# Performance work log

Measured on AMD Instinct MI355X. Metric: run time of the kernel, lower is better.

Reference implementation:

```python
import jax, jax.numpy as jnp
import numpy as np

DIM = 768
HEADS = 12
DIM_HEAD = 64
INNER = HEADS * DIM_HEAD  # 768
EPS = 1e-5


def setup_inputs() -> dict:
    key = jax.random.key(0)
    ks = jax.random.split(key, 5)
    x = jax.random.normal(ks[0], (4, 2048, DIM), dtype=jnp.float32)
    ln_g = jnp.ones((DIM,), dtype=jnp.float32)
    ln_b = jnp.zeros((DIM,), dtype=jnp.float32)
    s1 = 1.0 / np.sqrt(DIM)
    W_qkv = jax.random.uniform(ks[1], (DIM, 3 * INNER), dtype=jnp.float32, minval=-s1, maxval=s1)
    b_qkv = jax.random.uniform(ks[2], (3 * INNER,), dtype=jnp.float32, minval=-s1, maxval=s1)
    s2 = 1.0 / np.sqrt(INNER)
    W_out = jax.random.uniform(ks[3], (INNER, DIM), dtype=jnp.float32, minval=-s2, maxval=s2)
    b_out = jax.random.uniform(ks[4], (DIM,), dtype=jnp.float32, minval=-s2, maxval=s2)
    return {"x": x, "ln_g": ln_g, "ln_b": ln_b, "W_qkv": W_qkv, "b_qkv": b_qkv, "W_out": W_out, "b_out": b_out}


def reference(x, ln_g, ln_b, W_qkv, b_qkv, W_out, b_out):
    b, n, _ = x.shape
    # pre-norm LayerNorm
    mu = jnp.mean(x, axis=-1, keepdims=True)
    var = jnp.mean(jnp.square(x - mu), axis=-1, keepdims=True)
    xn = (x - mu) * jax.lax.rsqrt(var + EPS) * ln_g + ln_b
    qkv = xn @ W_qkv + b_qkv  # [b, n, 3*inner]
    q, k, v = jnp.split(qkv, 3, axis=-1)
    def to_heads(t):
        return t.reshape(b, n, HEADS, DIM_HEAD).transpose(0, 2, 1, 3)  # b h n d
    q, k, v = map(to_heads, (q, k, v))
    q = q * (DIM_HEAD ** -0.5)
    sim = jnp.einsum('bhid,bhjd->bhij', q, k)
    attn = jax.nn.softmax(sim, axis=-1)  # dropout is identity (p=0.0)
    out = jnp.einsum('bhij,bhjd->bhid', attn, v)
    out = out.transpose(0, 2, 1, 3).reshape(b, n, INNER)
    return out @ W_out + b_out
```

## Files before the change

### kernel.cpp

```cpp
#include <hip/hip_runtime.h>
#include <cstdint>
#include <cstddef>


#define SEQ    2048
#define NBATCH 4
#define DMODEL 768
#define NHEADS 12
#define DHEAD  64
#define MROWS  (NBATCH * SEQ)
#define NQKV   (3 * DMODEL)
#define KT     64
#define NT     (SEQ / KT)

using f32x4  = __attribute__((ext_vector_type(4))) float;
using u16x8  = __attribute__((ext_vector_type(8))) unsigned short;
using s16x8  = __attribute__((ext_vector_type(8))) short;

__device__ __forceinline__ unsigned short f2bf(float f) {
  union { float f; unsigned int u; } x; x.f = f;
  unsigned int r = x.u + 0x7fffu + ((x.u >> 16) & 1u);
  return (unsigned short)(r >> 16);
}

#if defined(__has_builtin)
#if __has_builtin(__builtin_amdgcn_cvt_pk_bf16_f32)
#define HAVE_PK_BF16 1
#endif
#if __has_builtin(__builtin_amdgcn_exp2f)
#define HAVE_EXP2 1
#endif
#endif

__device__ __forceinline__ unsigned int pk_bf16(float a, float b) {
#ifdef HAVE_PK_BF16
  auto v = __builtin_amdgcn_cvt_pk_bf16_f32(a, b);
  union { decltype(v) v2; unsigned int u; } c; c.v2 = v; return c.u;
#else
  return (unsigned int)f2bf(a) | ((unsigned int)f2bf(b) << 16);
#endif
}

__device__ __forceinline__ float fexp2(float x) {
#ifdef HAVE_EXP2
  return __builtin_amdgcn_exp2f(x);
#else
  return exp2f(x);
#endif
}

__device__ __forceinline__ f32x4 mfma16(u16x8 a, u16x8 b, f32x4 c) {
  return __builtin_amdgcn_mfma_f32_16x16x32_bf16((s16x8)a, (s16x8)b, c, 0, 0, 0);
}

__device__ __forceinline__ void gl_lds16(const void* g, void* l) {
  __builtin_amdgcn_global_load_lds(
      (const __attribute__((address_space(1))) void*)g,
      (__attribute__((address_space(3))) void*)l, 16, 0, 0);
}

__global__ __launch_bounds__(256) void ln_kernel(
    const float* __restrict__ x, const float* __restrict__ g,
    const float* __restrict__ bb, unsigned short* __restrict__ xn) {
  __shared__ float red[8];
  const int row = blockIdx.x, t = threadIdx.x;
  const float* xr = x + (size_t)row * DMODEL;
  float v0 = xr[t], v1 = xr[t + 256], v2 = xr[t + 512];
  float s = v0 + v1 + v2;
#pragma unroll
  for (int o = 32; o; o >>= 1) s += __shfl_down(s, o);
  if ((t & 63) == 0) red[t >> 6] = s;
  __syncthreads();
  float mu = (red[0] + red[1] + red[2] + red[3]) * (1.0f / DMODEL);
  float d0 = v0 - mu, d1 = v1 - mu, d2 = v2 - mu;
  float q = d0 * d0 + d1 * d1 + d2 * d2;
#pragma unroll
  for (int o = 32; o; o >>= 1) q += __shfl_down(q, o);
  if ((t & 63) == 0) red[4 + (t >> 6)] = q;
  __syncthreads();
  float var = (red[4] + red[5] + red[6] + red[7]) * (1.0f / DMODEL);
  float rstd = rsqrtf(var + 1e-5f);
  size_t base = (size_t)row * DMODEL;
  xn[base + t]       = f2bf(d0 * rstd * g[t]       + bb[t]);
  xn[base + t + 256] = f2bf(d1 * rstd * g[t + 256] + bb[t + 256]);
  xn[base + t + 512] = f2bf(d2 * rstd * g[t + 512] + bb[t + 512]);
}

__global__ __launch_bounds__(256) void tconv_kernel(
    const float* __restrict__ W, unsigned short* __restrict__ Wt, int N) {
  __shared__ float tile[32][33];
  const int n0 = blockIdx.x * 32, k0 = blockIdx.y * 32;
  const int tx = threadIdx.x & 31, ty = threadIdx.x >> 5;
#pragma unroll
  for (int r = 0; r < 4; ++r)
    tile[ty + r * 8][tx] = W[(size_t)(k0 + ty + r * 8) * N + n0 + tx];
  __syncthreads();
#pragma unroll
  for (int r = 0; r < 4; ++r)
    Wt[(size_t)(n0 + ty + r * 8) * DMODEL + k0 + tx] = f2bf(tile[tx][ty + r * 8]);
}

__global__ __launch_bounds__(256, 2) void gemm_qk_kernel(
    const unsigned short* __restrict__ Wt, const unsigned short* __restrict__ xn,
    const float* __restrict__ bias, unsigned short* __restrict__ qb,
    unsigned short* __restrict__ kb) {
  __shared__ alignas(16) unsigned short As[128 * 64];
  __shared__ alignas(16) unsigned short Bs[128 * 64];
  const int t = threadIdx.x, wid = t >> 6, l = t & 63, quad = l >> 4, ll = l & 15;
  const int a0 = blockIdx.x * 128;
  const int b0 = blockIdx.y * 128;
  const int wa = (wid >> 1) * 64, wb = (wid & 1) * 64;
  const int srow = l >> 3, sblk = (l & 7) ^ srow;
  f32x4 acc[4][4] = {};
  for (int k0 = 0; k0 < DMODEL; k0 += 64) {
#pragma unroll
    for (int cc = 0; cc < 4; ++cc) {
      int call = wid * 4 + cc;
      int r = call * 8 + srow;
      gl_lds16(Wt + (size_t)(a0 + r) * DMODEL + k0 + sblk * 8, &As[call * 512]);
      gl_lds16(xn + (size_t)(b0 + r) * DMODEL + k0 + sblk * 8, &Bs[call * 512]);
    }
    __syncthreads();
#pragma unroll
    for (int ks = 0; ks < 2; ++ks) {
      u16x8 af[4], bf[4];
#pragma unroll
      for (int i = 0; i < 4; ++i) {
        int ra = wa + i * 16 + ll, rb = wb + i * 16 + ll;
        int blk = (ks * 4 + quad) ^ (ll & 7);
        af[i] = *(const u16x8*)&As[ra * 64 + blk * 8];
        bf[i] = *(const u16x8*)&Bs[rb * 64 + blk * 8];
      }
#pragma unroll
      for (int mi = 0; mi < 4; ++mi)
#pragma unroll
        for (int ni = 0; ni < 4; ++ni)
          acc[mi][ni] = mfma16(af[mi], bf[ni], acc[mi][ni]);
    }
    __syncthreads();
  }
  const bool isq = (a0 < DMODEL);
  unsigned short* dst = isq ? qb : kb;
  const float sc = isq ? 0.18033688f : 1.0f;
#pragma unroll
  for (int mi = 0; mi < 4; ++mi) {
    int row0 = a0 + wa + mi * 16 + quad * 4;
    float4 bv = *(const float4*)&bias[row0];
    int rr = isq ? row0 : row0 - DMODEL;
    int h = rr >> 6, d0 = rr & 63;
#pragma unroll
    for (int ni = 0; ni < 4; ++ni) {
      int seq = b0 + wb + ni * 16 + ll;
      int b = seq >> 11, i = seq & 2047;
      uint2 pk;
      pk.x = pk_bf16((acc[mi][ni][0] + bv.x) * sc, (acc[mi][ni][1] + bv.y) * sc);
      pk.y = pk_bf16((acc[mi][ni][2] + bv.z) * sc, (acc[mi][ni][3] + bv.w) * sc);
      *(uint2*)&dst[(size_t)((b * NHEADS + h) * SEQ + i) * DHEAD + d0] = pk;
    }
  }
}

__global__ __launch_bounds__(256, 2) void gemm_v_kernel(
    const unsigned short* __restrict__ A, const unsigned short* __restrict__ Bt,
    const float* __restrict__ bias, unsigned short* __restrict__ vt) {
  __shared__ alignas(16) unsigned short As[128 * 64];
  __shared__ alignas(16) unsigned short Bs[128 * 64];
  const int t = threadIdx.x, wid = t >> 6, l = t & 63, quad = l >> 4, ll = l & 15;
  const int m0 = blockIdx.x * 128;
  const int n0 = 2 * DMODEL + blockIdx.y * 128;
  const int wm = (wid >> 1) * 64, wn = (wid & 1) * 64;
  const int srow = l >> 3, sblk = (l & 7) ^ srow;
  f32x4 acc[4][4] = {};
  for (int k0 = 0; k0 < DMODEL; k0 += 64) {
#pragma unroll
    for (int cc = 0; cc < 4; ++cc) {
      int call = wid * 4 + cc;
      int r = call * 8 + srow;
      gl_lds16(A  + (size_t)(m0 + r) * DMODEL + k0 + sblk * 8, &As[call * 512]);
      gl_lds16(Bt + (size_t)(n0 + r) * DMODEL + k0 + sblk * 8, &Bs[call * 512]);
    }
    __syncthreads();
#pragma unroll
    for (int ks = 0; ks < 2; ++ks) {
      u16x8 af[4], bf[4];
#pragma unroll
      for (int i = 0; i < 4; ++i) {
        int ra = wm + i * 16 + ll, rb = wn + i * 16 + ll;
        int blk = (ks * 4 + quad) ^ (ll & 7);
        af[i] = *(const u16x8*)&As[ra * 64 + blk * 8];
        bf[i] = *(const u16x8*)&Bs[rb * 64 + blk * 8];
      }
#pragma unroll
      for (int mi = 0; mi < 4; ++mi)
#pragma unroll
        for (int ni = 0; ni < 4; ++ni)
          acc[mi][ni] = mfma16(af[mi], bf[ni], acc[mi][ni]);
    }
    __syncthreads();
  }
#pragma unroll
  for (int mi = 0; mi < 4; ++mi) {
    int gm = m0 + wm + mi * 16 + quad * 4;
    int b = gm >> 11, i0 = gm & 2047;
#pragma unroll
    for (int ni = 0; ni < 4; ++ni) {
      int gn = n0 + wn + ni * 16 + ll;
      float bv = bias[gn];
      int rem = gn - 2 * DMODEL;
      int h = rem >> 6, d = rem & 63;
      int bh = b * NHEADS + h;
      uint2 pk;
      pk.x = pk_bf16(acc[mi][ni][0] + bv, acc[mi][ni][1] + bv);
      pk.y = pk_bf16(acc[mi][ni][2] + bv, acc[mi][ni][3] + bv);
      *(uint2*)&vt[((size_t)bh * DHEAD + d) * SEQ + i0] = pk;
    }
  }
}

__global__ __launch_bounds__(256, 3) void attn_kernel(
    const unsigned short* __restrict__ qbuf, const unsigned short* __restrict__ kbuf,
    const unsigned short* __restrict__ vtg, unsigned short* __restrict__ ao) {
  __shared__ alignas(16) unsigned short stage[2][2][KT * DHEAD];
  __shared__ alignas(16) unsigned short Pws[4][32 * 72];
  const int t = threadIdx.x, wid = t >> 6, l = t & 63, quad = l >> 4, ll = l & 15;
  const int qt = blockIdx.x, bh = blockIdx.y;
  const unsigned short* qg  = qbuf + ((size_t)bh * SEQ + qt * 128) * DHEAD;
  const unsigned short* kg0 = kbuf + (size_t)bh * SEQ * DHEAD;
  const unsigned short* vt0 = vtg  + (size_t)bh * DHEAD * SEQ;
  const int srow = l >> 3;
  const int sblk = (l & 7) ^ srow;

  unsigned short* Qs = &stage[0][0][0];
#pragma unroll
  for (int cc = 0; cc < 4; ++cc) {
    int call = wid * 4 + cc;
    gl_lds16(qg + (call * 8 + srow) * 64 + sblk * 8, Qs + call * 512);
  }
  __syncthreads();
  u16x8 qf[2][2];
#pragma unroll
  for (int mi = 0; mi < 2; ++mi)
#pragma unroll
    for (int ks = 0; ks < 2; ++ks) {
      int r = wid * 32 + mi * 16 + ll;
      int blk = (ks * 4 + quad) ^ (ll & 7);
      qf[mi][ks] = *(const u16x8*)&Qs[r * 64 + blk * 8];
    }
  __syncthreads();

  auto stage_tile = [&](int buf, int kt2) {
    const unsigned short* kg = kg0 + (size_t)kt2 * KT * DHEAD;
#pragma unroll
    for (int c = 0; c < 2; ++c) {
      int call = wid * 2 + c;
      int r = call * 8 + srow;
      gl_lds16(kg + r * 64 + sblk * 8, &stage[buf][0][call * 512]);
      gl_lds16(vt0 + (size_t)r * SEQ + kt2 * KT + sblk * 8, &stage[buf][1][call * 512]);
    }
  };

  f32x4 oacc[2][4] = {};
  float lsum[2] = {0.f, 0.f};
  unsigned short* Pw = Pws[wid];

  stage_tile(0, 0);
  int buf = 0;
  for (int kt2 = 0; kt2 < NT; ++kt2) {
    __syncthreads();
    if (kt2 + 1 < NT) stage_tile(buf ^ 1, kt2 + 1);
    const unsigned short* Ks = &stage[buf][0][0];
    const unsigned short* Vs = &stage[buf][1][0];

    f32x4 st[2][4] = {};
#pragma unroll
    for (int ks = 0; ks < 2; ++ks)
#pragma unroll
      for (int ni = 0; ni < 4; ++ni) {
        int r = ni * 16 + ll;
        int blk = (ks * 4 + quad) ^ (ll & 7);
        u16x8 kf = *(const u16x8*)&Ks[r * 64 + blk * 8];
        st[0][ni] = mfma16(kf, qf[0][ks], st[0][ni]);
        st[1][ni] = mfma16(kf, qf[1][ks], st[1][ni]);
      }

#pragma unroll
    for (int mi = 0; mi < 2; ++mi)
#pragma unroll
      for (int ni = 0; ni < 4; ++ni) {
        float p0 = fexp2(st[mi][ni][0]);
        float p1 = fexp2(st[mi][ni][1]);
        float p2 = fexp2(st[mi][ni][2]);
        float p3 = fexp2(st[mi][ni][3]);
        lsum[mi] += (p0 + p1) + (p2 + p3);
        uint2 pk;
        pk.x = pk_bf16(p0, p1);
        pk.y = pk_bf16(p2, p3);
        *(uint2*)&Pw[(mi * 16 + ll) * 72 + ni * 16 + quad * 4] = pk;
      }
    asm volatile("s_waitcnt lgkmcnt(0)" ::: "memory");

#pragma unroll
    for (int ks = 0; ks < 2; ++ks) {
      u16x8 pf0 = *(const u16x8*)&Pw[(ll) * 72 + ks * 32 + quad * 8];
      u16x8 pf1 = *(const u16x8*)&Pw[(16 + ll) * 72 + ks * 32 + quad * 8];
#pragma unroll
      for (int di = 0; di < 4; ++di) {
        int r = di * 16 + ll;
        int blk = (ks * 4 + quad) ^ (ll & 7);
        u16x8 vf = *(const u16x8*)&Vs[r * 64 + blk * 8];
        oacc[0][di] = mfma16(pf0, vf, oacc[0][di]);
        oacc[1][di] = mfma16(pf1, vf, oacc[1][di]);
      }
    }
    buf ^= 1;
  }

  float lsF[2];
#pragma unroll
  for (int mi = 0; mi < 2; ++mi) {
    float ls = lsum[mi];
    ls += __shfl_xor(ls, 16);
    ls += __shfl_xor(ls, 32);
    lsF[mi] = ls;
  }

  const int b = bh / NHEADS, h = bh - b * NHEADS;
#pragma unroll
  for (int mi = 0; mi < 2; ++mi) {
#pragma unroll
    for (int r = 0; r < 4; ++r) {
      float inv = 1.0f / __shfl(lsF[mi], quad * 4 + r);
      int row = qt * 128 + wid * 32 + mi * 16 + quad * 4 + r;
      size_t base = ((size_t)(b * SEQ + row)) * DMODEL + h * DHEAD;
#pragma unroll
      for (int di = 0; di < 4; ++di)
        ao[base + di * 16 + ll] = f2bf(oacc[mi][di][r] * inv);
    }
  }
}

__global__ __launch_bounds__(256, 2) void gemm_out_kernel(
    const unsigned short* __restrict__ Wt, const unsigned short* __restrict__ ao,
    const float* __restrict__ bias, float* __restrict__ out) {
  __shared__ alignas(16) unsigned short As[128 * 64];
  __shared__ alignas(16) unsigned short Bs[128 * 64];
  const int t = threadIdx.x, wid = t >> 6, l = t & 63, quad = l >> 4, ll = l & 15;
  const int a0 = blockIdx.x * 128;
  const int b0 = blockIdx.y * 128;
  const int wa = (wid >> 1) * 64, wb = (wid & 1) * 64;
  const int srow = l >> 3, sblk = (l & 7) ^ srow;
  f32x4 acc[4][4] = {};
  for (int k0 = 0; k0 < DMODEL; k0 += 64) {
#pragma unroll
    for (int cc = 0; cc < 4; ++cc) {
      int call = wid * 4 + cc;
      int r = call * 8 + srow;
      gl_lds16(Wt + (size_t)(a0 + r) * DMODEL + k0 + sblk * 8, &As[call * 512]);
      gl_lds16(ao + (size_t)(b0 + r) * DMODEL + k0 + sblk * 8, &Bs[call * 512]);
    }
    __syncthreads();
#pragma unroll
    for (int ks = 0; ks < 2; ++ks) {
      u16x8 af[4], bf[4];
#pragma unroll
      for (int i = 0; i < 4; ++i) {
        int ra = wa + i * 16 + ll, rb = wb + i * 16 + ll;
        int blk = (ks * 4 + quad) ^ (ll & 7);
        af[i] = *(const u16x8*)&As[ra * 64 + blk * 8];
        bf[i] = *(const u16x8*)&Bs[rb * 64 + blk * 8];
      }
#pragma unroll
      for (int mi = 0; mi < 4; ++mi)
#pragma unroll
        for (int ni = 0; ni < 4; ++ni)
          acc[mi][ni] = mfma16(af[mi], bf[ni], acc[mi][ni]);
    }
    __syncthreads();
  }
#pragma unroll
  for (int mi = 0; mi < 4; ++mi) {
    int row0 = a0 + wa + mi * 16 + quad * 4;
    float4 bv = *(const float4*)&bias[row0];
#pragma unroll
    for (int ni = 0; ni < 4; ++ni) {
      int seq = b0 + wb + ni * 16 + ll;
      float4 o;
      o.x = acc[mi][ni][0] + bv.x;
      o.y = acc[mi][ni][1] + bv.y;
      o.z = acc[mi][ni][2] + bv.z;
      o.w = acc[mi][ni][3] + bv.w;
      *(float4*)&out[(size_t)seq * DMODEL + row0] = o;
    }
  }
}

extern "C" void kernel_launch(void* const* d_in, const int* in_sizes, int n_in,
                              void* d_out, int out_size, void* d_ws, size_t ws_size,
                              hipStream_t stream) {
  const float* x     = (const float*)d_in[0];
  const float* ln_g  = (const float*)d_in[1];
  const float* ln_b  = (const float*)d_in[2];
  const float* W_qkv = (const float*)d_in[3];
  const float* b_qkv = (const float*)d_in[4];
  const float* W_out = (const float*)d_in[5];
  const float* b_out = (const float*)d_in[6];
  float* out = (float*)d_out;

  char* ws = (char*)d_ws;
  unsigned short* xn    = (unsigned short*)(ws);
  unsigned short* wqkvt = (unsigned short*)(ws + 12582912);
  unsigned short* woutt = (unsigned short*)(ws + 16121856);
  unsigned short* qb    = (unsigned short*)(ws + 17301504);
  unsigned short* kb    = (unsigned short*)(ws + 29884416);
  unsigned short* vt    = (unsigned short*)(ws + 42467328);
  unsigned short* ao    = xn;

  ln_kernel<<<MROWS, 256, 0, stream>>>(x, ln_g, ln_b, xn);
  tconv_kernel<<<dim3(NQKV / 32, DMODEL / 32), 256, 0, stream>>>(W_qkv, wqkvt, NQKV);
  tconv_kernel<<<dim3(DMODEL / 32, DMODEL / 32), 256, 0, stream>>>(W_out, woutt, DMODEL);
  gemm_qk_kernel<<<dim3(12, 64), 256, 0, stream>>>(wqkvt, xn, b_qkv, qb, kb);
  gemm_v_kernel<<<dim3(64, 6), 256, 0, stream>>>(xn, wqkvt, b_qkv, vt);
  attn_kernel<<<dim3(SEQ / 128, NBATCH * NHEADS), 256, 0, stream>>>(qb, kb, vt, ao);
  gemm_out_kernel<<<dim3(6, 64), 256, 0, stream>>>(woutt, ao, b_out, out);
}
```

Before: 240.2 us.

## Merge weight transposes and QKV GEMMs, reorder attention grid, shrink out-proj tile

The two weight transpose-convert launches become one kernel that picks its source by block index. The QK and V projection GEMMs become a single launch whose blocks branch on blockIdx.x to choose operand roles and epilogue layout. The attention grid is swapped so consecutive blocks take different batch-heads, which changes L2 locality for K/V. The output projection tile drops from 128 to 64 rows to double the block count (384 to 768) and improve occupancy, at the cost of less reuse per block.

```diff
diff --git a/kernel.cpp b/kernel.cpp
--- a/kernel.cpp
+++ b/kernel.cpp
@@ -86,10 +86,16 @@
   xn[base + t + 512] = f2bf(d2 * rstd * g[t + 512] + bb[t + 512]);
 }
 
-__global__ __launch_bounds__(256) void tconv_kernel(
-    const float* __restrict__ W, unsigned short* __restrict__ Wt, int N) {
+__global__ __launch_bounds__(256) void tconv_all_kernel(
+    const float* __restrict__ Wqkv, unsigned short* __restrict__ Wqkvt,
+    const float* __restrict__ Wout, unsigned short* __restrict__ Woutt) {
   __shared__ float tile[32][33];
-  const int n0 = blockIdx.x * 32, k0 = blockIdx.y * 32;
+  const int bx = blockIdx.x;
+  const bool isq = bx < 72;
+  const float* W = isq ? Wqkv : Wout;
+  unsigned short* Wt = isq ? Wqkvt : Woutt;
+  const int N = isq ? NQKV : DMODEL;
+  const int n0 = (isq ? bx : bx - 72) * 32, k0 = blockIdx.y * 32;
   const int tx = threadIdx.x & 31, ty = threadIdx.x >> 5;
 #pragma unroll
   for (int r = 0; r < 4; ++r)
@@ -100,15 +106,20 @@
     Wt[(size_t)(n0 + ty + r * 8) * DMODEL + k0 + tx] = f2bf(tile[tx][ty + r * 8]);
 }
 
-__global__ __launch_bounds__(256, 2) void gemm_qk_kernel(
+__global__ __launch_bounds__(256, 2) void gemm_qkv_kernel(
     const unsigned short* __restrict__ Wt, const unsigned short* __restrict__ xn,
     const float* __restrict__ bias, unsigned short* __restrict__ qb,
-    unsigned short* __restrict__ kb) {
+    unsigned short* __restrict__ kb, unsigned short* __restrict__ vt) {
   __shared__ alignas(16) unsigned short As[128 * 64];
   __shared__ alignas(16) unsigned short Bs[128 * 64];
   const int t = threadIdx.x, wid = t >> 6, l = t & 63, quad = l >> 4, ll = l & 15;
-  const int a0 = blockIdx.x * 128;
-  const int b0 = blockIdx.y * 128;
+  const int bx = blockIdx.x, by = blockIdx.y;
+  const bool isv = (bx >= 12);
+  const unsigned short* pA;
+  const unsigned short* pB;
+  int aBase, bBase;
+  if (!isv) { pA = Wt; aBase = bx * 128;  pB = xn; bBase = by * 128; }
+  else      { pA = xn; aBase = by * 128;  pB = Wt; bBase = 2 * DMODEL + (bx - 12) * 128; }
   const int wa = (wid >> 1) * 64, wb = (wid & 1) * 64;
   const int srow = l >> 3, sblk = (l & 7) ^ srow;
   f32x4 acc[4][4] = {};
@@ -117,8 +128,8 @@
     for (int cc = 0; cc < 4; ++cc) {
       int call = wid * 4 + cc;
       int r = call * 8 + srow;
-      gl_lds16(Wt + (size_t)(a0 + r) * DMODEL + k0 + sblk * 8, &As[call * 512]);
-      gl_lds16(xn + (size_t)(b0 + r) * DMODEL + k0 + sblk * 8, &Bs[call * 512]);
+      gl_lds16(pA + (size_t)(aBase + r) * DMODEL + k0 + sblk * 8, &As[call * 512]);
+      gl_lds16(pB + (size_t)(bBase + r) * DMODEL + k0 + sblk * 8, &Bs[call * 512]);
     }
     __syncthreads();
 #pragma unroll
@@ -139,80 +150,43 @@
     }
     __syncthreads();
   }
-  const bool isq = (a0 < DMODEL);
-  unsigned short* dst = isq ? qb : kb;
-  const float sc = isq ? 0.18033688f : 1.0f;
-#pragma unroll
-  for (int mi = 0; mi < 4; ++mi) {
-    int row0 = a0 + wa + mi * 16 + quad * 4;
-    float4 bv = *(const float4*)&bias[row0];
-    int rr = isq ? row0 : row0 - DMODEL;
-    int h = rr >> 6, d0 = rr & 63;
-#pragma unroll
-    for (int ni = 0; ni < 4; ++ni) {
-      int seq = b0 + wb + ni * 16 + ll;
-      int b = seq >> 11, i = seq & 2047;
-      uint2 pk;
-      pk.x = pk_bf16((acc[mi][ni][0] + bv.x) * sc, (acc[mi][ni][1] + bv.y) * sc);
-      pk.y = pk_bf16((acc[mi][ni][2] + bv.z) * sc, (acc[mi][ni][3] + bv.w) * sc);
-      *(uint2*)&dst[(size_t)((b * NHEADS + h) * SEQ + i) * DHEAD + d0] = pk;
-    }
-  }
-}
-
-__global__ __launch_bounds__(256, 2) void gemm_v_kernel(
-    const unsigned short* __restrict__ A, const unsigned short* __restrict__ Bt,
-    const float* __restrict__ bias, unsigned short* __restrict__ vt) {
-  __shared__ alignas(16) unsigned short As[128 * 64];
-  __shared__ alignas(16) unsigned short Bs[128 * 64];
-  const int t = threadIdx.x, wid = t >> 6, l = t & 63, quad = l >> 4, ll = l & 15;
-  const int m0 = blockIdx.x * 128;
-  const int n0 = 2 * DMODEL + blockIdx.y * 128;
-  const int wm = (wid >> 1) * 64, wn = (wid & 1) * 64;
-  const int srow = l >> 3, sblk = (l & 7) ^ srow;
-  f32x4 acc[4][4] = {};
-  for (int k0 = 0; k0 < DMODEL; k0 += 64) {
-#pragma unroll
-    for (int cc = 0; cc < 4; ++cc) {
-      int call = wid * 4 + cc;
-      int r = call * 8 + srow;
-      gl_lds16(A  + (size_t)(m0 + r) * DMODEL + k0 + sblk * 8, &As[call * 512]);
-      gl_lds16(Bt + (size_t)(n0 + r) * DMODEL + k0 + sblk * 8, &Bs[call * 512]);
-    }
-    __syncthreads();
-#pragma unroll
-    for (int ks = 0; ks < 2; ++ks) {
-      u16x8 af[4], bf[4];
-#pragma unroll
-      for (int i = 0; i < 4; ++i) {
-        int ra = wm + i * 16 + ll, rb = wn + i * 16 + ll;
-        int blk = (ks * 4 + quad) ^ (ll & 7);
-        af[i] = *(const u16x8*)&As[ra * 64 + blk * 8];
-        bf[i] = *(const u16x8*)&Bs[rb * 64 + blk * 8];
-      }
-#pragma unroll
-      for (int mi = 0; mi < 4; ++mi)
-#pragma unroll
-        for (int ni = 0; ni < 4; ++ni)
-          acc[mi][ni] = mfma16(af[mi], bf[ni], acc[mi][ni]);
-    }
-    __syncthreads();
-  }
-#pragma unroll
-  for (int mi = 0; mi < 4; ++mi) {
-    int gm = m0 + wm + mi * 16 + quad * 4;
-    int b = gm >> 11, i0 = gm & 2047;
-#pragma unroll
-    for (int ni = 0; ni < 4; ++ni) {
-      int gn = n0 + wn + ni * 16 + ll;
-      float bv = bias[gn];
-      int rem = gn - 2 * DMODEL;
-      int h = rem >> 6, d = rem & 63;
-      int bh = b * NHEADS + h;
-      uint2 pk;
-      pk.x = pk_bf16(acc[mi][ni][0] + bv, acc[mi][ni][1] + bv);
-      pk.y = pk_bf16(acc[mi][ni][2] + bv, acc[mi][ni][3] + bv);
-      *(uint2*)&vt[((size_t)bh * DHEAD + d) * SEQ + i0] = pk;
+  if (!isv) {
+    const bool isq = (aBase < DMODEL);
+    unsigned short* dst = isq ? qb : kb;
+    const float sc = isq ? 0.18033688f : 1.0f;
+#pragma unroll
+    for (int mi = 0; mi < 4; ++mi) {
+      int row0 = aBase + wa + mi * 16 + quad * 4;
+      float4 bv = *(const float4*)&bias[row0];
+      int rr = isq ? row0 : row0 - DMODEL;
+      int h = rr >> 6, d0 = rr & 63;
+#pragma unroll
+      for (int ni = 0; ni < 4; ++ni) {
+        int seq = bBase + wb + ni * 16 + ll;
+        int b = seq >> 11, i = seq & 2047;
+        uint2 pk;
+        pk.x = pk_bf16((acc[mi][ni][0] + bv.x) * sc, (acc[mi][ni][1] + bv.y) * sc);
+        pk.y = pk_bf16((acc[mi][ni][2] + bv.z) * sc, (acc[mi][ni][3] + bv.w) * sc);
+        *(uint2*)&dst[(size_t)((b * NHEADS + h) * SEQ + i) * DHEAD + d0] = pk;
+      }
+    }
+  } else {
+#pragma unroll
+    for (int mi = 0; mi < 4; ++mi) {
+      int gm = aBase + wa + mi * 16 + quad * 4;
+      int b = gm >> 11, i0 = gm & 2047;
+#pragma unroll
+      for (int ni = 0; ni < 4; ++ni) {
+        int gn = bBase + wb + ni * 16 + ll;
+        float bv = bias[gn];
+        int rem = gn - 2 * DMODEL;
+        int h = rem >> 6, d = rem & 63;
+        int bh = b * NHEADS + h;
+        uint2 pk;
+        pk.x = pk_bf16(acc[mi][ni][0] + bv, acc[mi][ni][1] + bv);
+        pk.y = pk_bf16(acc[mi][ni][2] + bv, acc[mi][ni][3] + bv);
+        *(uint2*)&vt[((size_t)bh * DHEAD + d) * SEQ + i0] = pk;
+      }
     }
   }
 }
@@ -223,7 +197,7 @@
   __shared__ alignas(16) unsigned short stage[2][2][KT * DHEAD];
   __shared__ alignas(16) unsigned short Pws[4][32 * 72];
   const int t = threadIdx.x, wid = t >> 6, l = t & 63, quad = l >> 4, ll = l & 15;
-  const int qt = blockIdx.x, bh = blockIdx.y;
+  const int bh = blockIdx.x, qt = blockIdx.y;
   const unsigned short* qg  = qbuf + ((size_t)bh * SEQ + qt * 128) * DHEAD;
   const unsigned short* kg0 = kbuf + (size_t)bh * SEQ * DHEAD;
   const unsigned short* vt0 = vtg  + (size_t)bh * DHEAD * SEQ;
@@ -342,35 +316,45 @@
 __global__ __launch_bounds__(256, 2) void gemm_out_kernel(
     const unsigned short* __restrict__ Wt, const unsigned short* __restrict__ ao,
     const float* __restrict__ bias, float* __restrict__ out) {
-  __shared__ alignas(16) unsigned short As[128 * 64];
+  __shared__ alignas(16) unsigned short As[64 * 64];
   __shared__ alignas(16) unsigned short Bs[128 * 64];
   const int t = threadIdx.x, wid = t >> 6, l = t & 63, quad = l >> 4, ll = l & 15;
-  const int a0 = blockIdx.x * 128;
+  const int a0 = blockIdx.x * 64;
   const int b0 = blockIdx.y * 128;
-  const int wa = (wid >> 1) * 64, wb = (wid & 1) * 64;
+  const int wa = (wid >> 1) * 32, wb = (wid & 1) * 64;
   const int srow = l >> 3, sblk = (l & 7) ^ srow;
-  f32x4 acc[4][4] = {};
+  f32x4 acc[2][4] = {};
   for (int k0 = 0; k0 < DMODEL; k0 += 64) {
+#pragma unroll
+    for (int cc = 0; cc < 2; ++cc) {
+      int call = wid * 2 + cc;
+      int r = call * 8 + srow;
+      gl_lds16(Wt + (size_t)(a0 + r) * DMODEL + k0 + sblk * 8, &As[call * 512]);
+    }
 #pragma unroll
     for (int cc = 0; cc < 4; ++cc) {
       int call = wid * 4 + cc;
       int r = call * 8 + srow;
-      gl_lds16(Wt + (size_t)(a0 + r) * DMODEL + k0 + sblk * 8, &As[call * 512]);
       gl_lds16(ao + (size_t)(b0 + r) * DMODEL + k0 + sblk * 8, &Bs[call * 512]);
     }
     __syncthreads();
 #pragma unroll
     for (int ks = 0; ks < 2; ++ks) {
-      u16x8 af[4], bf[4];
-#pragma unroll
-      for (int i = 0; i < 4; ++i) {
-        int ra = wa + i * 16 + ll, rb = wb + i * 16 + ll;
+      u16x8 af[2], bf[4];
+#pragma unroll
+      for (int i = 0; i < 2; ++i) {
+        int ra = wa + i * 16 + ll;
         int blk = (ks * 4 + quad) ^ (ll & 7);
         af[i] = *(const u16x8*)&As[ra * 64 + blk * 8];
+      }
+#pragma unroll
+      for (int i = 0; i < 4; ++i) {
+        int rb = wb + i * 16 + ll;
+        int blk = (ks * 4 + quad) ^ (ll & 7);
         bf[i] = *(const u16x8*)&Bs[rb * 64 + blk * 8];
       }
 #pragma unroll
-      for (int mi = 0; mi < 4; ++mi)
+      for (int mi = 0; mi < 2; ++mi)
 #pragma unroll
         for (int ni = 0; ni < 4; ++ni)
           acc[mi][ni] = mfma16(af[mi], bf[ni], acc[mi][ni]);
@@ -378,7 +362,7 @@
     __syncthreads();
   }
 #pragma unroll
-  for (int mi = 0; mi < 4; ++mi) {
+  for (int mi = 0; mi < 2; ++mi) {
     int row0 = a0 + wa + mi * 16 + quad * 4;
     float4 bv = *(const float4*)&bias[row0];
 #pragma unroll
@@ -416,10 +400,8 @@
   unsigned short* ao    = xn;
 
   ln_kernel<<<MROWS, 256, 0, stream>>>(x, ln_g, ln_b, xn);
-  tconv_kernel<<<dim3(NQKV / 32, DMODEL / 32), 256, 0, stream>>>(W_qkv, wqkvt, NQKV);
-  tconv_kernel<<<dim3(DMODEL / 32, DMODEL / 32), 256, 0, stream>>>(W_out, woutt, DMODEL);
-  gemm_qk_kernel<<<dim3(12, 64), 256, 0, stream>>>(wqkvt, xn, b_qkv, qb, kb);
-  gemm_v_kernel<<<dim3(64, 6), 256, 0, stream>>>(xn, wqkvt, b_qkv, vt);
-  attn_kernel<<<dim3(SEQ / 128, NBATCH * NHEADS), 256, 0, stream>>>(qb, kb, vt, ao);
-  gemm_out_kernel<<<dim3(6, 64), 256, 0, stream>>>(woutt, ao, b_out, out);
-}
+  tconv_all_kernel<<<dim3(96, 24), 256, 0, stream>>>(W_qkv, wqkvt, W_out, woutt);
+  gemm_qkv_kernel<<<dim3(18, 64), 256, 0, stream>>>(wqkvt, xn, b_qkv, qb, kb, vt);
+  attn_kernel<<<dim3(NBATCH * NHEADS, SEQ / 128), 256, 0, stream>>>(qb, kb, vt, ao);
+  gemm_out_kernel<<<dim3(12, 64), 256, 0, stream>>>(woutt, ao, b_out, out);
+}
```

Result: slower. 252.4 us (+5.1%).
